# Kernel optimization log

Measured on AMD Instinct MI355X. Metric: run time of the kernel, lower is better.

The kernel has to match this reference:

```python
import jax, jax.numpy as jnp
import numpy as np

H = 8  # num_heads


def setup_inputs() -> dict:
    key = jax.random.key(0)
    ks = jax.random.split(key, 10)
    B, N, C_sp, C_fd = 16, 4096, 768, 512
    s = 0.02
    return {
        "spatial_tokens": jax.random.normal(ks[0], (B, N, C_sp), jnp.float32),
        "freq_token": jax.random.normal(ks[1], (B, C_fd), jnp.float32),
        "Wq": jax.random.normal(ks[2], (C_sp, C_sp), jnp.float32) * s,
        "bq": jax.random.normal(ks[3], (C_sp,), jnp.float32) * s,
        "Wk": jax.random.normal(ks[4], (C_sp, C_fd), jnp.float32) * s,
        "bk": jax.random.normal(ks[5], (C_sp,), jnp.float32) * s,
        "Wv": jax.random.normal(ks[6], (C_sp, C_fd), jnp.float32) * s,
        "bv": jax.random.normal(ks[7], (C_sp,), jnp.float32) * s,
        "Wo": jax.random.normal(ks[8], (C_sp, C_sp), jnp.float32) * s,
        "bo": jax.random.normal(ks[9], (C_sp,), jnp.float32) * s,
    }


def reference(spatial_tokens, freq_token, Wq, bq, Wk, bk, Wv, bv, Wo, bo):
    B, N, C = spatial_tokens.shape
    D = C // H  # head_dim
    scale = jnp.sqrt(jnp.float32(D))
    # projections (torch Linear: x @ W.T + b)
    Q = spatial_tokens @ Wq.T + bq                 # [B, N, C]
    K = freq_token @ Wk.T + bk                     # [B, C] (single KV token)
    V = freq_token @ Wv.T + bv                     # [B, C]
    Qh = Q.reshape(B, N, H, D).transpose(0, 2, 1, 3)   # [B, H, N, D]
    Kh = K.reshape(B, 1, H, D).transpose(0, 2, 1, 3)   # [B, H, 1, D]
    Vh = V.reshape(B, 1, H, D).transpose(0, 2, 1, 3)   # [B, H, 1, D]
    scores = jnp.einsum('bhnd,bhkd->bhnk', Qh, Kh) / scale  # [B, H, N, 1]
    weights = jax.nn.softmax(scores, axis=-1)                # all-ones (k=1)
    attn = jnp.einsum('bhnk,bhkd->bhnd', weights, Vh)        # [B, H, N, D]
    attn = attn.transpose(0, 2, 1, 3).reshape(B, N, C)
    return attn @ Wo.T + bo                        # [B, N, C]
```

## Files before the change

kernel.cpp:

```cpp
#include <hip/hip_runtime.h>
#include <hip/hip_bf16.h>


#define B_   16
#define N_   4096
#define CSP  768
#define CFD  512

__global__ void __launch_bounds__(128) compute_v(const float* __restrict__ freq,
                                                 const float* __restrict__ Wv,
                                                 const float* __restrict__ bv,
                                                 float* __restrict__ V) {
    const int b   = blockIdx.x;
    const int tid = threadIdx.x;
    const int j   = blockIdx.y * 128 + tid;

    __shared__ float4 sF[CFD / 4];
    sF[tid] = ((const float4*)(freq + (size_t)b * CFD))[tid];
    __syncthreads();

    float acc = bv[j];
    const float4* wr = (const float4*)Wv + (size_t)j * (CFD / 4);
#pragma unroll 4
    for (int i = 0; i < CFD / 4; ++i) {
        float4 w = wr[i];
        float4 f = sF[i];
        acc += w.x * f.x + w.y * f.y + w.z * f.z + w.w * f.w;
    }
    V[(size_t)b * CSP + j] = acc;
}

__global__ void __launch_bounds__(128) compute_o2(const float* __restrict__ V,
                                                  const float* __restrict__ Wo,
                                                  const float* __restrict__ bo,
                                                  float* __restrict__ O2) {
    const int b   = blockIdx.x;
    const int tid = threadIdx.x;
    const int c   = blockIdx.y * 128 + tid;

    __shared__ float4 sV[CSP / 4];
    for (int i = tid; i < CSP / 4; i += 128)
        sV[i] = ((const float4*)(V + (size_t)b * CSP))[i];
    __syncthreads();

    float acc = bo[c];
    const float4* wr = (const float4*)Wo + (size_t)c * (CSP / 4);
#pragma unroll 4
    for (int i = 0; i < CSP / 4; ++i) {
        float4 w = wr[i];
        float4 v = sV[i];
        acc += w.x * v.x + w.y * v.y + w.z * v.z + w.w * v.w;
    }
    O2[(size_t)b * CSP + c] = acc;
}

#define ROWS 32
__global__ void __launch_bounds__(192) broadcast_out(const float* __restrict__ O2,
                                                     float* __restrict__ out) {
    const int b     = blockIdx.x;
    const int chunk = blockIdx.y;
    const int tid   = threadIdx.x;

    const float4 v = ((const float4*)(O2 + (size_t)b * CSP))[tid];

    float4* dst = (float4*)(out + ((size_t)b * N_ + (size_t)chunk * ROWS) * CSP) + tid;
#pragma unroll
    for (int r = 0; r < ROWS; ++r) {
        dst[(size_t)r * (CSP / 4)] = v;
    }
}

extern "C" void kernel_launch(void* const* d_in, const int* in_sizes, int n_in,
                              void* d_out, int out_size, void* d_ws, size_t ws_size,
                              hipStream_t stream) {
    const float* freq = (const float*)d_in[1];
    const float* Wv   = (const float*)d_in[6];
    const float* bv   = (const float*)d_in[7];
    const float* Wo   = (const float*)d_in[8];
    const float* bo   = (const float*)d_in[9];
    float* out = (float*)d_out;

    float* V  = (float*)d_ws;
    float* O2 = V + (size_t)B_ * CSP;

    compute_v <<<dim3(B_, CSP / 128), 128, 0, stream>>>(freq, Wv, bv, V);
    compute_o2<<<dim3(B_, CSP / 128), 128, 0, stream>>>(V, Wo, bo, O2);
    broadcast_out<<<dim3(B_, N_ / ROWS), 192, 0, stream>>>(O2, out);
}
```

Baseline: 348.8 us.

## Fuse V projection, output projection and broadcast into one kernel

Merges the three kernels (V projection, output projection, row broadcast) into a single kernel. Each block recomputes V and O2 for its batch in shared memory and then writes 256 rows of the broadcast output. This removes two kernel launches and the workspace round trip. In exchange, every one of the 16 chunks per batch repeats the two small GEMVs, re-reading Wv and Wo many times, which adds a serial compute phase before the stores.

```diff
diff --git a/kernel.cpp b/kernel.cpp
--- a/kernel.cpp
+++ b/kernel.cpp
@@ -2,72 +2,68 @@
 #include <hip/hip_bf16.h>
 
 
-#define B_   16
-#define N_   4096
-#define CSP  768
-#define CFD  512
+#define B_    16
+#define N_    4096
+#define CSP   768
+#define CFD   512
+#define ROWS_PER_BLK 256
+#define TPB   768
 
-__global__ void __launch_bounds__(128) compute_v(const float* __restrict__ freq,
-                                                 const float* __restrict__ Wv,
-                                                 const float* __restrict__ bv,
-                                                 float* __restrict__ V) {
-    const int b   = blockIdx.x;
-    const int tid = threadIdx.x;
-    const int j   = blockIdx.y * 128 + tid;
+__global__ void __launch_bounds__(TPB) fused_cross_attn(
+    const float* __restrict__ freq,
+    const float* __restrict__ Wv,
+    const float* __restrict__ bv,
+    const float* __restrict__ Wo,
+    const float* __restrict__ bo,
+    float* __restrict__ out)
+{
+    const int b     = blockIdx.x;
+    const int chunk = blockIdx.y;
+    const int t     = threadIdx.x;
 
-    __shared__ float4 sF[CFD / 4];
-    sF[tid] = ((const float4*)(freq + (size_t)b * CFD))[tid];
+    __shared__ __align__(16) float sF[CFD];
+    __shared__ __align__(16) float sV[CSP];
+    __shared__ __align__(16) float sO[CSP];
+
+    if (t < CFD) sF[t] = freq[(size_t)b * CFD + t];
     __syncthreads();
 
-    float acc = bv[j];
-    const float4* wr = (const float4*)Wv + (size_t)j * (CFD / 4);
-#pragma unroll 4
-    for (int i = 0; i < CFD / 4; ++i) {
-        float4 w = wr[i];
-        float4 f = sF[i];
-        acc += w.x * f.x + w.y * f.y + w.z * f.z + w.w * f.w;
+    {
+        float acc = bv[t];
+        const float4* wr = (const float4*)Wv + (size_t)t * (CFD / 4);
+        const float4* fr = (const float4*)sF;
+#pragma unroll 8
+        for (int i = 0; i < CFD / 4; ++i) {
+            float4 w = wr[i];
+            float4 f = fr[i];
+            acc += w.x * f.x + w.y * f.y + w.z * f.z + w.w * f.w;
+        }
+        sV[t] = acc;
     }
-    V[(size_t)b * CSP + j] = acc;
-}
-
-__global__ void __launch_bounds__(128) compute_o2(const float* __restrict__ V,
-                                                  const float* __restrict__ Wo,
-                                                  const float* __restrict__ bo,
-                                                  float* __restrict__ O2) {
-    const int b   = blockIdx.x;
-    const int tid = threadIdx.x;
-    const int c   = blockIdx.y * 128 + tid;
-
-    __shared__ float4 sV[CSP / 4];
-    for (int i = tid; i < CSP / 4; i += 128)
-        sV[i] = ((const float4*)(V + (size_t)b * CSP))[i];
     __syncthreads();
 
-    float acc = bo[c];
-    const float4* wr = (const float4*)Wo + (size_t)c * (CSP / 4);
-#pragma unroll 4
-    for (int i = 0; i < CSP / 4; ++i) {
-        float4 w = wr[i];
-        float4 v = sV[i];
-        acc += w.x * v.x + w.y * v.y + w.z * v.z + w.w * v.w;
+    {
+        float acc = bo[t];
+        const float4* wr = (const float4*)Wo + (size_t)t * (CSP / 4);
+        const float4* vr = (const float4*)sV;
+#pragma unroll 8
+        for (int i = 0; i < CSP / 4; ++i) {
+            float4 w = wr[i];
+            float4 v = vr[i];
+            acc += w.x * v.x + w.y * v.y + w.z * v.z + w.w * v.w;
+        }
+        sO[t] = acc;
     }
-    O2[(size_t)b * CSP + c] = acc;
-}
+    __syncthreads();
 
-#define ROWS 32
-__global__ void __launch_bounds__(192) broadcast_out(const float* __restrict__ O2,
-                                                     float* __restrict__ out) {
-    const int b     = blockIdx.x;
-    const int chunk = blockIdx.y;
-    const int tid   = threadIdx.x;
+    const int col4 = t % (CSP / 4);
+    const int r0   = t / (CSP / 4);
+    const float4 v = ((const float4*)sO)[col4];
 
-    const float4 v = ((const float4*)(O2 + (size_t)b * CSP))[tid];
-
-    float4* dst = (float4*)(out + ((size_t)b * N_ + (size_t)chunk * ROWS) * CSP) + tid;
-#pragma unroll
-    for (int r = 0; r < ROWS; ++r) {
+    float4* dst = (float4*)(out + ((size_t)b * N_ + (size_t)chunk * ROWS_PER_BLK) * CSP) + col4;
+#pragma unroll 8
+    for (int r = r0; r < ROWS_PER_BLK; r += 4)
         dst[(size_t)r * (CSP / 4)] = v;
-    }
 }
 
 extern "C" void kernel_launch(void* const* d_in, const int* in_sizes, int n_in,
@@ -80,10 +76,6 @@
     const float* bo   = (const float*)d_in[9];
     float* out = (float*)d_out;
 
-    float* V  = (float*)d_ws;
-    float* O2 = V + (size_t)B_ * CSP;
-
-    compute_v <<<dim3(B_, CSP / 128), 128, 0, stream>>>(freq, Wv, bv, V);
-    compute_o2<<<dim3(B_, CSP / 128), 128, 0, stream>>>(V, Wo, bo, O2);
-    broadcast_out<<<dim3(B_, N_ / ROWS), 192, 0, stream>>>(O2, out);
+    fused_cross_attn<<<dim3(B_, N_ / ROWS_PER_BLK), TPB, 0, stream>>>(
+        freq, Wv, bv, Wo, bo, out);
 }
```

Result: slower. 416.6 us (+19.4%).
